# Performance work log

Hardware: AMD Instinct MI355X
Metric: run time of the kernel (lower is better)

## Reference

```python
import jax, jax.numpy as jnp
import numpy as np

E = 65536; N = 10000; LAT = 128; K = 8; OH = 128; GD = 64
M0, M1, M2 = 64, 32, 16                 # multiplicities of 0e, 1o, 2e
D_EDGE = M0 + 3 * M1 + 5 * M2           # 240
NG = M1 + M2                            # 48 gate scalars
O0 = M0 + NG                            # 112 scalar outputs of SO2 (scalars + gates)
C0, C1, C2 = 3 * M0, 3 * M1, 3 * M2     # per-l channels of cat(node, edge, node)
FIN0 = C0 + C1 + C2                     # 336 channels at m=0
FIN1 = C1 + C2                          # 144 channels at |m|=1
FIN2 = C2                               # 48 channels at |m|=2
OUT0 = O0 + M1 + M2                     # 160


def _silu(x):
    return x * jax.nn.sigmoid(x)


def _mlp(x, Ws, bs):
    for i, (W, b) in enumerate(zip(Ws, bs)):
        x = x @ W + b
        if i < len(Ws) - 1:
            x = _silu(x)
    return x


def _split(f):
    # [*, 240] -> scalars [*,64], l1 [*,32,3], l2 [*,16,5]
    return (f[:, :M0],
            f[:, M0:M0 + 3 * M1].reshape(-1, M1, 3),
            f[:, M0 + 3 * M1:].reshape(-1, M2, 5))


def forward(latents, node_features, node_onehot, edge_features, edge_vector,
            cutoff_coeffs, edge_one_hot, wigner_D1, wigner_D2, mole_globals,
            Wg, W0, W1r, W1i, W2r, W2i, P0, b0, P1, P2, We, be, ln_g, ln_b,
            M1W0, M1b0, M1W1, M1b1, M1W2, M1b2,
            M2W0, M2b0, M2W1, M2b1, M2W2, M2b2,
            T0, T1, T2, edge_index, active_edges):
    ec = edge_index[0][active_edges]
    en = edge_index[1][active_edges]
    nc = node_features[ec]
    nnb = node_features[en]
    lat_a = latents[active_edges]

    nc0, nc1, nc2 = _split(nc)
    ef0, ef1, ef2 = _split(edge_features)
    nn0, nn1, nn2 = _split(nnb)
    x0 = jnp.concatenate([nc0, ef0, nn0], 1)          # [E,192]
    x1 = jnp.concatenate([nc1, ef1, nn1], 1)          # [E,96,3]
    x2 = jnp.concatenate([nc2, ef2, nn2], 1)          # [E,48,5]

    # rotate into the edge-aligned frame with cached Wigner D matrices
    y1 = jnp.einsum('eij,ecj->eci', wigner_D1, x1)
    y2 = jnp.einsum('eij,ecj->eci', wigner_D2, x2)

    # expert gates: softmax over routed experts + always-on shared expert
    g = jax.nn.softmax(mole_globals @ Wg, axis=-1)    # [E,K]
    gf = jnp.concatenate([g, jnp.ones((g.shape[0], 1), g.dtype)], 1)  # [E,K+1]

    def moe(f, W):  # f [E,F], W [K+1,F,O] -> gated mixture of expert linears
        return jnp.einsum('eko,ek->eo', jnp.einsum('ef,kfo->eko', f, W), gf)

    # SO(2) linear: independent mixing per |m|
    f0 = jnp.concatenate([x0, y1[:, :, 1], y2[:, :, 2]], 1)   # [E,336]
    o0 = moe(f0, W0)                                          # [E,160]
    o0_s, o0_1, o0_2 = o0[:, :O0], o0[:, O0:O0 + M1], o0[:, O0 + M1:]
    fp1 = jnp.concatenate([y1[:, :, 2], y2[:, :, 3]], 1)      # [E,144]
    fm1 = jnp.concatenate([y1[:, :, 0], y2[:, :, 1]], 1)
    op1 = moe(fp1, W1r) - moe(fm1, W1i)                       # [E,48]
    om1 = moe(fp1, W1i) + moe(fm1, W1r)
    fp2, fm2 = y2[:, :, 4], y2[:, :, 0]                       # [E,48]
    op2 = moe(fp2, W2r) - moe(fm2, W2i)                       # [E,16]
    om2 = moe(fp2, W2i) + moe(fm2, W2r)

    z1 = jnp.stack([om1[:, :M1], o0_1, op1[:, :M1]], -1)      # [E,32,3]
    z2 = jnp.stack([om2, om1[:, M1:], o0_2, op1[:, M1:], op2], -1)  # [E,16,5]
    z1 = jnp.einsum('eji,ecj->eci', wigner_D1, z1)            # rotate back (D^T)
    z2 = jnp.einsum('eji,ecj->eci', wigner_D2, z2)

    # Gate activation: silu scalars, sigmoid gates multiply l>0 parts
    sc = _silu(o0_s[:, :M0])
    gates = jax.nn.sigmoid(o0_s[:, M0:])
    v1 = z1 * gates[:, :M1, None]
    v2 = z2 * gates[:, M1:, None]

    # lin_post: per-l channel mixing, bias on scalars only
    sc = sc @ P0 + b0
    v1 = jnp.einsum('ecm,cd->edm', v1, P1)
    v2 = jnp.einsum('ecm,cd->edm', v2, P2)
    scalars = sc                                              # [E,64]

    # E3ElementLinear: per-channel weights generated from latents
    w = lat_a @ We + be                                       # [E,112]
    sc = sc * w[:, :M0]
    v1 = v1 * w[:, M0:M0 + M1, None]
    v2 = v2 * w[:, M0 + M1:, None]
    new_edge = jnp.concatenate([sc, v1.reshape(-1, 3 * M1), v2.reshape(-1, 5 * M2)], 1)

    # latent update: LN -> MLP1(cat scalars) -> MLP2(cat one-hot) -> cutoff
    mu = lat_a.mean(-1, keepdims=True)
    var = ((lat_a - mu) ** 2).mean(-1, keepdims=True)
    ln = (lat_a - mu) * jax.lax.rsqrt(var + 1e-5) * ln_g + ln_b
    nl = _mlp(jnp.concatenate([ln, scalars], 1), [M1W0, M1W1, M1W2], [M1b0, M1b1, M1b2])
    nl = _mlp(jnp.concatenate([nl, edge_one_hot], 1), [M2W0, M2W1, M2W2], [M2b0, M2b1, M2b2])
    nl = cutoff_coeffs[active_edges][:, None] * nl

    # residual update (identity res since irreps_in == irreps_out)
    upd = jax.nn.sigmoid(jnp.zeros((), new_edge.dtype))
    c_old = jax.lax.rsqrt(upd * upd + 1.0)
    c_new = upd * c_old
    edge_out = c_old * edge_features + c_new * new_edge
    latents = latents.at[active_edges].set(c_new * nl + c_old * lat_a)

    # edge one-hot tensor product (uvu, weighted): per-channel scale from one-hot
    s = 1.0 / jnp.sqrt(jnp.asarray(OH, new_edge.dtype))
    t0 = (edge_one_hot @ T0.T) * s                            # [E,64]
    t1 = (edge_one_hot @ T1.T) * s                            # [E,32]
    t2 = (edge_one_hot @ T2.T) * s                            # [E,16]
    e0, e1, e2 = _split(edge_out)
    oh = jnp.concatenate([e0 * t0,
                          (e1 * t1[:, :, None]).reshape(-1, 3 * M1),
                          (e2 * t2[:, :, None]).reshape(-1, 5 * M2)], 1)
    edge_out = edge_out + oh
    return edge_out, latents, wigner_D1, wigner_D2


def setup_inputs():
    key = jax.random.key(0)
    ks = iter(jax.random.split(key, 64))

    def rn(shape, scale=1.0):
        return jax.random.normal(next(ks), shape, dtype=jnp.float32) * scale

    d = {}
    d['latents'] = rn((E, LAT))
    d['node_features'] = rn((N, D_EDGE))
    d['node_onehot'] = rn((N, GD))
    d['edge_features'] = rn((E, D_EDGE))
    ev = rn((E, 3))
    d['edge_vector'] = ev / jnp.linalg.norm(ev, axis=-1, keepdims=True)
    d['cutoff_coeffs'] = jax.random.uniform(next(ks), (E,), dtype=jnp.float32)
    d['edge_one_hot'] = rn((E, OH))
    d['wigner_D1'] = rn((E, 3, 3), 1.0 / np.sqrt(3))
    d['wigner_D2'] = rn((E, 5, 5), 1.0 / np.sqrt(5))
    d['mole_globals'] = rn((E, GD))
    d['edge_index'] = jax.random.randint(next(ks), (2, E), 0, N, dtype=jnp.int32)
    d['active_edges'] = jnp.arange(E, dtype=jnp.int32)
    # parameters
    d['Wg'] = rn((GD, K), 1.0 / np.sqrt(GD))
    d['W0'] = rn((K + 1, FIN0, OUT0), 1.0 / np.sqrt(FIN0))
    d['W1r'] = rn((K + 1, FIN1, NG), 1.0 / np.sqrt(FIN1))
    d['W1i'] = rn((K + 1, FIN1, NG), 1.0 / np.sqrt(FIN1))
    d['W2r'] = rn((K + 1, FIN2, M2), 1.0 / np.sqrt(FIN2))
    d['W2i'] = rn((K + 1, FIN2, M2), 1.0 / np.sqrt(FIN2))
    d['P0'] = rn((M0, M0), 1.0 / np.sqrt(M0)); d['b0'] = jnp.zeros((M0,), jnp.float32)
    d['P1'] = rn((M1, M1), 1.0 / np.sqrt(M1))
    d['P2'] = rn((M2, M2), 1.0 / np.sqrt(M2))
    d['We'] = rn((LAT, M0 + M1 + M2), 1.0 / np.sqrt(LAT))
    d['be'] = jnp.zeros((M0 + M1 + M2,), jnp.float32)
    d['ln_g'] = jnp.ones((LAT,), jnp.float32); d['ln_b'] = jnp.zeros((LAT,), jnp.float32)
    d['M1W0'] = rn((LAT + M0, 128), 1.0 / np.sqrt(LAT + M0)); d['M1b0'] = jnp.zeros((128,), jnp.float32)
    d['M1W1'] = rn((128, 128), 1.0 / np.sqrt(128)); d['M1b1'] = jnp.zeros((128,), jnp.float32)
    d['M1W2'] = rn((128, LAT), 1.0 / np.sqrt(128)); d['M1b2'] = jnp.zeros((LAT,), jnp.float32)
    d['M2W0'] = rn((LAT + OH, 128), 1.0 / np.sqrt(LAT + OH)); d['M2b0'] = jnp.zeros((128,), jnp.float32)
    d['M2W1'] = rn((128, 128), 1.0 / np.sqrt(128)); d['M2b1'] = jnp.zeros((128,), jnp.float32)
    d['M2W2'] = rn((128, LAT), 1.0 / np.sqrt(128)); d['M2b2'] = jnp.zeros((LAT,), jnp.float32)
    d['T0'] = rn((M0, OH), 1.0 / np.sqrt(OH))
    d['T1'] = rn((M1, OH), 1.0 / np.sqrt(OH))
    d['T2'] = rn((M2, OH), 1.0 / np.sqrt(OH))
    return d


def reference(latents, node_features, node_onehot, edge_features, edge_vector,
              cutoff_coeffs, edge_one_hot, wigner_D1, wigner_D2, mole_globals,
              Wg, W0, W1r, W1i, W2r, W2i, P0, b0, P1, P2, We, be, ln_g, ln_b,
              M1W0, M1b0, M1W1, M1b1, M1W2, M1b2,
              M2W0, M2b0, M2W1, M2b1, M2W2, M2b2,
              T0, T1, T2, edge_index, active_edges):
    return forward(latents, node_features, node_onehot, edge_features, edge_vector,
                   cutoff_coeffs, edge_one_hot, wigner_D1, wigner_D2, mole_globals,
                   Wg, W0, W1r, W1i, W2r, W2i, P0, b0, P1, P2, We, be, ln_g, ln_b,
                   M1W0, M1b0, M1W1, M1b1, M1W2, M1b2,
                   M2W0, M2b0, M2W1, M2b1, M2W2, M2b2,
                   T0, T1, T2, edge_index, active_edges)
```

## Files before the change

### kernel.cpp

```cpp
#include <hip/hip_runtime.h>
#include <hip/hip_bf16.h>
#include <stdint.h>

#define EDGES 65536

typedef unsigned int uint;
typedef unsigned short ushort;
using bf16x8 = __attribute__((ext_vector_type(8))) __bf16;
using f32x4  = __attribute__((ext_vector_type(4))) float;
using uintx4 = __attribute__((ext_vector_type(4))) uint;
using float4v = __attribute__((ext_vector_type(4))) float;
using float2v = __attribute__((ext_vector_type(2))) float;

#define C_OLD 0.8944271909999159f
#define C_NEW 0.4472135954999579f
#define T_SCALE 0.08838834764831845f

__device__ __forceinline__ ushort f2bf(float f) {
  uint x = __builtin_bit_cast(uint, f);
  uint r = x + 0x7FFFu + ((x >> 16) & 1u);
  return (ushort)(r >> 16);
}
__device__ __forceinline__ float bf2f(ushort u) {
  uint x = (uint)u << 16;
  return __builtin_bit_cast(float, x);
}
__device__ __forceinline__ void gload16(const void* g, void* l) {
  __builtin_amdgcn_global_load_lds(
      (const __attribute__((address_space(1))) void*)g,
      (__attribute__((address_space(3))) void*)l, 16, 0, 0);
}

struct PackArgs {
  const float *W0, *W1r, *W1i, *W2r, *W2i;
  const float *s0, *s1, *s2, *s3, *s4, *s5, *we, *t0, *t1, *t2, *p0;
  ushort *B0, *B1, *B2;
  ushort *d0, *d1, *d2, *d3, *d4, *d5, *dwe, *dtt, *dp0;
};
__global__ __launch_bounds__(256) void k_pack(PackArgs p) {
  int bid = blockIdx.x;
  if (bid < 2160) {
    int idx = bid * 256 + threadIdx.x;
    if (idx >= 160 * 3456) return;
    int o = idx / 3456, kf = idx - o * 3456;
    int k = kf / 384, f = kf - k * 384;
    float v = (f < 336) ? p.W0[k * 53760 + f * 160 + o] : 0.f;
    p.B0[idx] = f2bf(v);
  } else if (bid < 3240) {
    int idx = (bid - 2160) * 256 + threadIdx.x;
    if (idx >= 96 * 2880) return;
    int c = idx / 2880, kf = idx - c * 2880;
    int k = kf / 320, f = kf - k * 320;
    float v = 0.f;
    if (f < 288) {
      if (c < 48) v = (f < 144) ? p.W1r[k * 6912 + f * 48 + c] : -p.W1i[k * 6912 + (f - 144) * 48 + c];
      else        v = (f < 144) ? p.W1i[k * 6912 + f * 48 + (c - 48)] : p.W1r[k * 6912 + (f - 144) * 48 + (c - 48)];
    }
    p.B1[idx] = f2bf(v);
  } else if (bid < 3384) {
    int idx = (bid - 3240) * 256 + threadIdx.x;
    if (idx >= 32 * 1152) return;
    int c = idx / 1152, kf = idx - c * 1152;
    int k = kf / 128, f = kf - k * 128;
    float v = 0.f;
    if (f < 96) {
      if (c < 16) v = (f < 48) ? p.W2r[k * 768 + f * 16 + c] : -p.W2i[k * 768 + (f - 48) * 16 + c];
      else        v = (f < 48) ? p.W2i[k * 768 + f * 16 + (c - 16)] : p.W2r[k * 768 + (f - 48) * 16 + (c - 16)];
    }
    p.B2[idx] = f2bf(v);
  } else {
    int idx = (bid - 3384) * 256 + threadIdx.x;
    if (idx < 24576) {
      int n = idx / 192, k = idx - n * 192;
      p.d0[idx] = f2bf(p.s0[k * 128 + n]);
    } else if (idx < 40960) {
      int q = idx - 24576; int n = q >> 7, k = q & 127;
      p.d1[q] = f2bf(p.s1[k * 128 + n]);
    } else if (idx < 57344) {
      int q = idx - 40960; int n = q >> 7, k = q & 127;
      p.d2[q] = f2bf(p.s2[k * 128 + n]);
    } else if (idx < 90112) {
      int q = idx - 57344; int n = q / 256, k = q - n * 256;
      p.d3[q] = f2bf(p.s3[k * 128 + n]);
    } else if (idx < 106496) {
      int q = idx - 90112; int n = q >> 7, k = q & 127;
      p.d4[q] = f2bf(p.s4[k * 128 + n]);
    } else if (idx < 122880) {
      int q = idx - 106496; int n = q >> 7, k = q & 127;
      p.d5[q] = f2bf(p.s5[k * 128 + n]);
    } else if (idx < 139264) {
      int q = idx - 122880; int n = q >> 7, k = q & 127;
      p.dwe[q] = f2bf((n < 112) ? p.we[k * 112 + n] : 0.f);
    } else if (idx < 155648) {
      int q = idx - 139264; int o = q >> 7, h = q & 127;
      float v = 0.f;
      if (o < 64) v = p.t0[o * 128 + h];
      else if (o < 96) v = p.t1[(o - 64) * 128 + h];
      else if (o < 112) v = p.t2[(o - 96) * 128 + h];
      p.dtt[q] = f2bf(v);
    } else if (idx < 159744) {
      int q = idx - 155648; int n = q >> 6, k = q & 63;
      p.dp0[q] = f2bf(p.p0[k * 64 + n]);
    }
  }
}

__global__ __launch_bounds__(256) void k_prep(
    const float* __restrict__ node_f, const float* __restrict__ edge_f,
    const float* __restrict__ D1g, const float* __restrict__ D2g,
    const float* __restrict__ mg_g, const float* __restrict__ Wg,
    const float* __restrict__ latg, const float* __restrict__ eohg,
    const int* __restrict__ eidx, const int* __restrict__ act,
    ushort* __restrict__ f_all, float* __restrict__ gf_out,
    ushort* __restrict__ lat_bf, ushort* __restrict__ mlp2_in) {
  __shared__ float sh[4][1244];
  const int w = threadIdx.x >> 6, lane = threadIdx.x & 63;
  const int e = blockIdx.x * 4 + w;
  float* s = sh[w];
  float* s_nc = s;
  float* s_ef = s + 240;
  float* s_nn = s + 480;
  float* s_d1 = s + 720;
  float* s_d2 = s + 729;
  float* s_mg = s + 754;
  float* s_lg = s + 818;
  ushort* row = (ushort*)(s + 828);
  const int ae = act[e];
  const int ec = eidx[ae], en = eidx[EDGES + ae];
  if (lane < 60) {
    ((float4v*)s_nc)[lane] = ((const float4v*)(node_f + (size_t)ec * 240))[lane];
    ((float4v*)s_ef)[lane] = ((const float4v*)(edge_f + (size_t)e * 240))[lane];
    ((float4v*)s_nn)[lane] = ((const float4v*)(node_f + (size_t)en * 240))[lane];
  }
  if (lane < 9)  s_d1[lane] = D1g[e * 9 + lane];
  if (lane < 25) s_d2[lane] = D2g[e * 25 + lane];
  s_mg[lane] = mg_g[e * 64 + lane];
  {
    const float* lp = latg + (size_t)ae * 128;
    float a0 = lp[2 * lane], a1 = lp[2 * lane + 1];
    ((uint*)lat_bf)[(size_t)e * 64 + lane] = (uint)f2bf(a0) | ((uint)f2bf(a1) << 16);
    const float* ep = eohg + (size_t)e * 128;
    a0 = ep[2 * lane]; a1 = ep[2 * lane + 1];
    ((uint*)mlp2_in)[(size_t)e * 128 + 64 + lane] = (uint)f2bf(a0) | ((uint)f2bf(a1) << 16);
  }
  {
    int k = lane & 7, hg = lane >> 3;
    float a = 0.f;
#pragma unroll
    for (int h = 0; h < 8; ++h) a += s_mg[hg * 8 + h] * Wg[(hg * 8 + h) * 8 + k];
    a += __shfl_xor(a, 8);
    a += __shfl_xor(a, 16);
    a += __shfl_xor(a, 32);
    if (lane < 8) s_lg[lane] = a;
  }
  if (lane < 12) {
    float m = s_lg[0];
    for (int j = 1; j < 8; ++j) m = fmaxf(m, s_lg[j]);
    float den = 0.f;
    for (int j = 0; j < 8; ++j) den += __expf(s_lg[j] - m);
    float v = 0.f;
    if (lane < 8) v = __expf(s_lg[lane] - m) / den;
    else if (lane == 8) v = 1.f;
    gf_out[e * 12 + lane] = v;
  }
  row[lane]       = f2bf(s_nc[lane]);
  row[64 + lane]  = f2bf(s_ef[lane]);
  row[128 + lane] = f2bf(s_nn[lane]);
  if (lane < 48) row[336 + lane] = 0;
  if (lane < 32) { row[672 + lane] = 0; row[800 + lane] = 0; }
#pragma unroll
  for (int it = 0; it < 5; ++it) {
    int q = lane + it * 64;
    if (q < 288) {
      int i = q / 96, c = q - i * 96;
      const float* src = (c < 32) ? s_nc : (c < 64) ? s_ef : s_nn;
      int base = 64 + (c & 31) * 3;
      float v = s_d1[i * 3] * src[base] + s_d1[i * 3 + 1] * src[base + 1] + s_d1[i * 3 + 2] * src[base + 2];
      int dst = (i == 0) ? 528 : (i == 1) ? 192 : 384;
      row[dst + c] = f2bf(v);
    }
  }
#pragma unroll
  for (int it = 0; it < 4; ++it) {
    int q = lane + it * 64;
    if (q < 240) {
      int i = q / 48, c = q - i * 48;
      const float* src = (c < 16) ? s_nc : (c < 32) ? s_ef : s_nn;
      int base = 160 + (c & 15) * 5;
      float v = s_d2[i * 5] * src[base] + s_d2[i * 5 + 1] * src[base + 1] +
                s_d2[i * 5 + 2] * src[base + 2] + s_d2[i * 5 + 3] * src[base + 3] +
                s_d2[i * 5 + 4] * src[base + 4];
      int dst = (i == 0) ? 752 : (i == 1) ? 624 : (i == 2) ? 288 : (i == 3) ? 480 : 704;
      row[dst + c] = f2bf(v);
    }
  }
  const uintx4* row4 = (const uintx4*)row;
  uintx4* dst4 = (uintx4*)(f_all + (size_t)e * 832);
#pragma unroll
  for (int it = 0; it < 2; ++it) {
    int q = lane + it * 64;
    if (q < 104) dst4[q] = row4[q];
  }
}

template <int WAVES, int BM, int KZP, int SPG2, int NGRP, int NCOL, int FOFF, int ASTRIDE,
          bool HASBIAS, int EPI>
__device__ __forceinline__ void gemm_dev(
    int bid, char* sm,
    const ushort* __restrict__ A, const ushort* __restrict__ Bt,
    const float* __restrict__ gf, const float* __restrict__ bias,
    ushort* __restrict__ outb, int ob_stride, int ob_off,
    ushort* __restrict__ outb2) {
  constexpr int T = WAVES * 64;
  constexpr int WRS = WAVES / 2;
  constexpr int RPW = BM / WRS;
  constexpr int MI = RPW / 16;
  constexpr int NFW = NCOL / 32;
  constexpr int A_BYTES = BM * 128;
  constexpr int B_BYTES = NCOL * 128;
  constexpr int NT2 = KZP / 64;
  constexpr int AI = (BM * 8) / T;
  constexpr int NB = NCOL * 8;
  constexpr int BI = (NB + T - 1) / T;
  static_assert(NCOL % 32 == 0 && KZP % 64 == 0 && RPW % 16 == 0 && (BM * 8) % T == 0, "geom");
  const int tid = threadIdx.x;
  const int lane = tid & 63, wid = tid >> 6;
  const int wr = wid >> 1, wc = wid & 1;
  const int g16 = lane >> 4;
  const int lane15 = lane & 15;
  const int e0 = bid * BM;
  const f32x4 vzero = {0.f, 0.f, 0.f, 0.f};

  const char* bSrc[BI];
#pragma unroll
  for (int it = 0; it < BI; ++it) {
    int q = tid + it * T;
    if (q < NB) {
      int c = q >> 3, ch = (q & 7) ^ (c & 7);
      bSrc[it] = (const char*)(Bt + (size_t)c * KZP) + ch * 16;
    } else bSrc[it] = nullptr;
  }

  f32x4 accS[MI][NFW];
#pragma unroll
  for (int mi = 0; mi < MI; ++mi)
#pragma unroll
    for (int n = 0; n < NFW; ++n) accS[mi][n] = vzero;

  if constexpr (NGRP > 1) {
    char* b_lds = sm;
    f32x4 accC[MI][NFW];
#pragma unroll
    for (int mi = 0; mi < MI; ++mi)
#pragma unroll
      for (int n = 0; n < NFW; ++n) accC[mi][n] = vzero;

    float gfr[MI][4];
    auto gf_pref = [&](int gx) {
#pragma unroll
      for (int mi = 0; mi < MI; ++mi)
#pragma unroll
        for (int j = 0; j < 4; ++j)
          gfr[mi][j] = gf[(size_t)(e0 + wr * RPW + mi * 16 + g16 * 4 + j) * 12 + gx];
    };
    gf_pref(0);

    bf16x8 afr[SPG2][MI][2];
#pragma unroll
    for (int wi = 0; wi < SPG2; ++wi)
#pragma unroll
      for (int mi = 0; mi < MI; ++mi)
#pragma unroll
        for (int s = 0; s < 2; ++s)
          afr[wi][mi][s] = *(const bf16x8*)(
              A + (size_t)(e0 + wr * RPW + mi * 16 + lane15) * ASTRIDE + FOFF +
              wi * 64 + s * 32 + g16 * 8);

    auto stageB = [&](int t2, int buf) {
#pragma unroll
      for (int it = 0; it < BI; ++it) {
        int q = tid + it * T;
        if (q < NB)
          gload16(bSrc[it] + (size_t)t2 * 128, b_lds + buf * B_BYTES + (tid - lane + it * T) * 16);
      }
    };

    stageB(0, 0);
    __syncthreads();
    int cur = 0;
    for (int g = 0; g < NGRP; ++g) {
#pragma unroll
      for (int wi = 0; wi < SPG2; ++wi) {
        int t2 = g * SPG2 + wi;
        if (t2 + 1 < NT2) stageB(t2 + 1, cur ^ 1);
        const char* bL = b_lds + cur * B_BYTES;
#pragma unroll
        for (int s = 0; s < 2; ++s) {
#pragma unroll
          for (int n = 0; n < NFW; ++n) {
            int cB = (wc * NFW + n) * 16 + lane15;
            int slot = (s * 4 + g16) ^ (cB & 7);
            bf16x8 b = *(const bf16x8*)(bL + cB * 128 + slot * 16);
#pragma unroll
            for (int mi = 0; mi < MI; ++mi)
              accC[mi][n] = __builtin_amdgcn_mfma_f32_16x16x32_bf16(afr[wi][mi][s], b, accC[mi][n], 0, 0, 0);
          }
        }
        if (wi == SPG2 - 1) {
#pragma unroll
          for (int mi = 0; mi < MI; ++mi)
#pragma unroll
            for (int n = 0; n < NFW; ++n) {
#pragma unroll
              for (int j = 0; j < 4; ++j) accS[mi][n][j] += gfr[mi][j] * accC[mi][n][j];
              accC[mi][n] = vzero;
            }
          if (g + 1 < NGRP) gf_pref(g + 1);
        }
        __syncthreads();
        cur ^= 1;
      }
    }
  } else {
    char* a_lds = sm;
    char* b_lds = sm + 2 * A_BYTES;
    const char* aSrc[AI];
#pragma unroll
    for (int it = 0; it < AI; ++it) {
      int q = tid + it * T;
      int r = q >> 3, ch = (q & 7) ^ (r & 7);
      aSrc[it] = (const char*)(A + (size_t)(e0 + r) * ASTRIDE + FOFF) + ch * 16;
    }
    auto stage = [&](int t2, int buf) {
#pragma unroll
      for (int it = 0; it < AI; ++it)
        gload16(aSrc[it] + t2 * 128, a_lds + buf * A_BYTES + (tid - lane + it * T) * 16);
#pragma unroll
      for (int it = 0; it < BI; ++it) {
        int q = tid + it * T;
        if (q < NB)
          gload16(bSrc[it] + t2 * 128, b_lds + buf * B_BYTES + (tid - lane + it * T) * 16);
      }
    };
    stage(0, 0);
    __syncthreads();
    int cur = 0;
    for (int t2 = 0; t2 < NT2; ++t2) {
      if (t2 + 1 < NT2) stage(t2 + 1, cur ^ 1);
      const char* aL = a_lds + cur * A_BYTES;
      const char* bL = b_lds + cur * B_BYTES;
#pragma unroll
      for (int s = 0; s < 2; ++s) {
        bf16x8 a[MI];
#pragma unroll
        for (int mi = 0; mi < MI; ++mi) {
          int rA = wr * RPW + mi * 16 + lane15;
          int slot = (s * 4 + g16) ^ (rA & 7);
          a[mi] = *(const bf16x8*)(aL + rA * 128 + slot * 16);
        }
#pragma unroll
        for (int n = 0; n < NFW; ++n) {
          int cB = (wc * NFW + n) * 16 + lane15;
          int slot = (s * 4 + g16) ^ (cB & 7);
          bf16x8 b = *(const bf16x8*)(bL + cB * 128 + slot * 16);
#pragma unroll
          for (int mi = 0; mi < MI; ++mi)
            accS[mi][n] = __builtin_amdgcn_mfma_f32_16x16x32_bf16(a[mi], b, accS[mi][n], 0, 0, 0);
        }
      }
      __syncthreads();
      cur ^= 1;
    }
  }

#pragma unroll
  for (int mi = 0; mi < MI; ++mi) {
    const int row0 = wr * RPW + mi * 16 + g16 * 4;
#pragma unroll
    for (int n = 0; n < NFW; ++n) {
      const int c = (wc * NFW + n) * 16 + lane15;
      float bv = 0.f;
      if constexpr (HASBIAS) bv = bias[c];
#pragma unroll
      for (int j = 0; j < 4; ++j) {
        float v = accS[mi][n][j] + bv;
        const int er = e0 + row0 + j;
        if constexpr (EPI == 1) v = v / (1.f + __expf(-v));
        outb[(size_t)er * ob_stride + ob_off + c] = f2bf(v);
        if constexpr (EPI == 2) {
          if ((wc * NFW + n) * 16 < 64)
            outb2[(size_t)er * 256 + c] = f2bf(v / (1.f + __expf(-v)));
        }
      }
    }
  }
}

struct MoeArgs {
  const ushort *f_all, *B0t, *B1t, *B2t;
  const float* gfb;
  ushort *moeout, *m2in;
};
__global__ __launch_bounds__(512) void k_moe(MoeArgs a) {
  __shared__ char sm[2 * 160 * 128 + 16];
  int bid = blockIdx.x;
  if (bid < 512) {
    gemm_dev<8, 128, 3456, 6, 9, 160, 0, 832, false, 2>(
        bid, sm, a.f_all, a.B0t, a.gfb, nullptr, a.moeout, 288, 0, a.m2in);
  } else if (bid < 1024) {
    gemm_dev<8, 128, 2880, 5, 9, 96, 384, 832, false, 0>(
        bid - 512, sm, a.f_all, a.B1t, a.gfb, nullptr, a.moeout, 288, 160, nullptr);
  } else {
    gemm_dev<8, 128, 1152, 2, 9, 32, 704, 832, false, 0>(
        bid - 1024, sm, a.f_all, a.B2t, a.gfb, nullptr, a.moeout, 288, 256, nullptr);
  }
}

struct Small3Args {
  const ushort *latbf, *Wet, *m2in, *Ttb, *P0t;
  const float* b0;
  ushort *wbuf, *tbuf, *m1in;
};
__global__ __launch_bounds__(256) void k_small3(Small3Args a) {
  __shared__ char sm[49168];
  int bid = blockIdx.x;
  if (bid < 1024) {
    gemm_dev<4, 64, 128, 1, 1, 128, 0, 128, false, 0>(
        bid, sm, a.latbf, a.Wet, nullptr, nullptr, a.wbuf, 128, 0, nullptr);
  } else if (bid < 2048) {
    gemm_dev<4, 64, 128, 1, 1, 128, 128, 256, false, 0>(
        bid - 1024, sm, a.m2in, a.Ttb, nullptr, nullptr, a.tbuf, 128, 0, nullptr);
  } else {
    gemm_dev<4, 64, 64, 1, 1, 64, 0, 256, true, 0>(
        bid - 2048, sm, a.m2in, a.P0t, nullptr, a.b0, a.m1in, 192, 128, nullptr);
  }
}

struct MlpArgs {
  const ushort *m1in, *m2in, *Wt1, *Wt2, *Wt3, *Wt4, *Wt5, *Wt6;
  const float *b1, *b2, *b3, *b4, *b5, *b6;
  const int* act;
  const float *cutg, *latg;
  float* out_lat;
};
__global__ __launch_bounds__(256) void k_mlp(MlpArgs A) {
  __shared__ char sm[61440];
  char* Xa = sm;
  char* Xb = sm + 12288;
  char* Xe = sm + 20480;
  char* W0 = sm + 28672;
  char* W1 = sm + 45056;
  const int tid = threadIdx.x;
  const int lane = tid & 63, w = tid >> 6;
  const int wr = w >> 1, wc = w & 1;
  const int lane15 = lane & 15, g16 = lane >> 4;
  const int e32 = blockIdx.x * 32;
  const f32x4 vzero = {0.f, 0.f, 0.f, 0.f};

  auto stage_w = [&](const ushort* Wt, int K2, int t2, char* dst) {
#pragma unroll
    for (int it = 0; it < 4; ++it) {
      int q = tid + it * 256;
      int c = q >> 3, ch = (q & 7) ^ (c & 7);
      gload16((const char*)Wt + (size_t)c * K2 + t2 * 128 + ch * 16,
              dst + (w + it * 4) * 1024);
    }
  };
  {
#pragma unroll
    for (int it = 0; it < 3; ++it) {
      int q = tid + it * 256;
      int r = q / 24, c24 = q - r * 24;
      int t2 = c24 >> 3, ch = (c24 & 7) ^ (r & 7);
      gload16((const char*)A.m1in + (size_t)(e32 + r) * 384 + t2 * 128 + ch * 16,
              Xa + (w + it * 4) * 1024);
    }
#pragma unroll
    for (int it = 0; it < 2; ++it) {
      int q = tid + it * 256;
      int r = q >> 4, c16 = q & 15;
      int t2 = c16 >> 3, ch = (c16 & 7) ^ (r & 7);
      gload16((const char*)A.m2in + (size_t)(e32 + r) * 512 + 256 + t2 * 128 + ch * 16,
              Xe + (w + it * 4) * 1024);
    }
  }
  stage_w(A.Wt1, 384, 0, W0);
  __syncthreads();

  f32x4 acc[4];
#pragma unroll
  for (int n = 0; n < 4; ++n) acc[n] = vzero;

  auto compute = [&](const char* xin, int xstride, int t2loc, const char* wl) {
#pragma unroll
    for (int s = 0; s < 2; ++s) {
      int row = wr * 16 + lane15;
      bf16x8 a = *(const bf16x8*)(xin + row * xstride + t2loc * 128 + (((s * 4 + g16) ^ (row & 7)) << 4));
#pragma unroll
      for (int n = 0; n < 4; ++n) {
        int cB = wc * 64 + n * 16 + lane15;
        bf16x8 b = *(const bf16x8*)(wl + cB * 128 + (((s * 4 + g16) ^ (cB & 7)) << 4));
        acc[n] = __builtin_amdgcn_mfma_f32_16x16x32_bf16(a, b, acc[n], 0, 0, 0);
      }
    }
  };
  auto epi_x = [&](const float* bias, char* xout, int xstride, bool dosilu) {
#pragma unroll
    for (int n = 0; n < 4; ++n) {
      int c = wc * 64 + n * 16 + lane15;
      float bv = bias[c];
      int ch = (n * 16 + lane15) >> 3;
#pragma unroll
      for (int j = 0; j < 4; ++j) {
        int row = wr * 16 + g16 * 4 + j;
        float v = acc[n][j] + bv;
        if (dosilu) v = v / (1.f + __expf(-v));
        *(ushort*)(xout + row * xstride + wc * 128 + ((ch ^ (row & 7)) << 4) + ((lane15 & 7) << 1)) = f2bf(v);
      }
      acc[n] = vzero;
    }
  };

  stage_w(A.Wt1, 384, 1, W1); compute(Xa, 384, 0, W0); __syncthreads();
  stage_w(A.Wt1, 384, 2, W0); compute(Xa, 384, 1, W1); __syncthreads();
  stage_w(A.Wt2, 256, 0, W1); compute(Xa, 384, 2, W0); epi_x(A.b1, Xb, 256, true); __syncthreads();
  stage_w(A.Wt2, 256, 1, W0); compute(Xb, 256, 0, W1); __syncthreads();
  stage_w(A.Wt3, 256, 0, W1); compute(Xb, 256, 1, W0); epi_x(A.b2, Xa, 384, true); __syncthreads();
  stage_w(A.Wt3, 256, 1, W0); compute(Xa, 384, 0, W1); __syncthreads();
  stage_w(A.Wt4, 512, 0, W1); compute(Xa, 384, 1, W0); epi_x(A.b3, Xb, 256, false); __syncthreads();
  stage_w(A.Wt4, 512, 1, W0); compute(Xb, 256, 0, W1); __syncthreads();
  stage_w(A.Wt4, 512, 2, W1); compute(Xb, 256, 1, W0); __syncthreads();
  stage_w(A.Wt4, 512, 3, W0); compute(Xe, 256, 0, W1); __syncthreads();
  stage_w(A.Wt5, 256, 0, W1); compute(Xe, 256, 1, W0); epi_x(A.b4, Xa, 384, true); __syncthreads();
  stage_w(A.Wt5, 256, 1, W0); compute(Xa, 384, 0, W1); __syncthreads();
  stage_w(A.Wt6, 256, 0, W1); compute(Xa, 384, 1, W0); epi_x(A.b5, Xb, 256, true); __syncthreads();
  stage_w(A.Wt6, 256, 1, W0); compute(Xb, 256, 0, W1); __syncthreads();
  compute(Xb, 256, 1, W0);
#pragma unroll
  for (int n = 0; n < 4; ++n) {
    int c = wc * 64 + n * 16 + lane15;
    float bv = A.b6[c];
#pragma unroll
    for (int j = 0; j < 4; ++j) {
      int row = wr * 16 + g16 * 4 + j;
      int er = e32 + row;
      int ae = A.act[er];
      float v = acc[n][j] + bv;
      A.out_lat[(size_t)ae * 128 + c] = C_NEW * A.cutg[ae] * v + C_OLD * A.latg[(size_t)ae * 128 + c];
    }
  }
}

__global__ __launch_bounds__(512) void k_postf(
    const ushort* __restrict__ moeout,
    const float* __restrict__ D1g, const float* __restrict__ D2g,
    const float* __restrict__ latg, const int* __restrict__ act,
    const float* __restrict__ P1, const float* __restrict__ P2,
    const ushort* __restrict__ wbuf, const float* __restrict__ beg,
    const float* __restrict__ lng, const float* __restrict__ lnb,
    const ushort* __restrict__ tbufp, const float* __restrict__ efg,
    ushort* __restrict__ m1in, float* __restrict__ out_edge) {
  __shared__ float SM[1136 + 8 * 920];
  ushort* Btab = (ushort*)SM;
  float* be_s = SM + 768;
  float* lng_s = SM + 880;
  float* lnb_s = SM + 1008;
  const int t = threadIdx.x;
  const int w = t >> 6, lane = t & 63;
  float* Wp = SM + 1136 + w * 920;
  float* o   = Wp;
  float* row = Wp + 224;
  float* sg  = Wp + 464;
  float* d1  = Wp + 512;
  float* d2  = Wp + 524;
  ushort* wvh = (ushort*)(Wp + 552);
  ushort* tvh = (ushort*)(Wp + 608);
  ushort* tile = (ushort*)(Wp + 664);
  const int e = blockIdx.x * 8 + w;
  const int ae = act[e];
  const f32x4 vzero = {0.f, 0.f, 0.f, 0.f};

  float ef[4];
  ef[0] = efg[(size_t)e * 240 + lane];
  ef[1] = efg[(size_t)e * 240 + 64 + lane];
  ef[2] = efg[(size_t)e * 240 + 128 + lane];
  ef[3] = (lane < 48) ? efg[(size_t)e * 240 + 192 + lane] : 0.f;
  float2v ll = ((const float2v*)(latg + (size_t)ae * 128))[lane];

  if (lane < 28) {
    uintx4 raw = *(const uintx4*)(moeout + (size_t)e * 288 + 64 + lane * 8);
    float* dst = o + lane * 8;
#pragma unroll
    for (int j = 0; j < 4; ++j) {
      uint u = raw[j];
      dst[2 * j] = bf2f((ushort)(u & 0xFFFF));
      dst[2 * j + 1] = bf2f((ushort)(u >> 16));
    }
  }
  if (lane < 14) {
    *(uintx4*)((char*)wvh + lane * 16) = *(const uintx4*)(wbuf + (size_t)e * 128 + lane * 8);
    *(uintx4*)((char*)tvh + lane * 16) = *(const uintx4*)(tbufp + (size_t)e * 128 + lane * 8);
  }
  if (lane < 8) {
    uintx4 raw = *(const uintx4*)(m1in + (size_t)e * 192 + 128 + lane * 8);
    float* dst = row + lane * 8;
#pragma unroll
    for (int j = 0; j < 4; ++j) {
      uint u = raw[j];
      dst[2 * j] = bf2f((ushort)(u & 0xFFFF));
      dst[2 * j + 1] = bf2f((ushort)(u >> 16));
    }
  }
  if (lane < 9)  d1[lane] = D1g[(size_t)e * 9 + lane];
  if (lane < 25) d2[lane] = D2g[(size_t)e * 25 + lane];
  if (lane < 48) sg[lane] = 1.f / (1.f + __expf(-o[lane]));

#pragma unroll
  for (int i = 0; i < 3; ++i) {
    int q = t + i * 512;
    int tbl = q >> 9, idx = q & 511;
    int d = idx >> 5, c = idx & 31;
    float v;
    if (tbl == 0) v = P1[c * 32 + d];
    else if (tbl == 1) v = P1[c * 32 + 16 + d];
    else v = (c < 16) ? P2[c * 16 + d] : 0.f;
    Btab[tbl * 512 + d * 32 + (((c >> 3) ^ (d & 3)) << 3) + (c & 7)] = f2bf(v);
  }
  if (t < 368) {
    if (t < 112) be_s[t] = beg[t];
    else if (t < 240) lng_s[t - 112] = lng[t - 112];
    else lnb_s[t - 240] = lnb[t - 240];
  }

  float sum = ll[0] + ll[1];
  float sq = ll[0] * ll[0] + ll[1] * ll[1];
#pragma unroll
  for (int m = 32; m > 0; m >>= 1) {
    sum += __shfl_xor(sum, m);
    sq += __shfl_xor(sq, m);
  }
  const float mu = sum * (1.f / 128.f);
  const float rs = rsqrtf(sq * (1.f / 128.f) - mu * mu + 1e-5f);

  __syncthreads();

  {
    int i = 2 * lane;
    float l0 = (ll[0] - mu) * rs * lng_s[i] + lnb_s[i];
    float l1 = (ll[1] - mu) * rs * lng_s[i + 1] + lnb_s[i + 1];
    ((uint*)m1in)[(size_t)e * 96 + lane] = (uint)f2bf(l0) | ((uint)f2bf(l1) << 16);
  }
#pragma unroll
  for (int rr = 0; rr < 2; ++rr) {
    int r = lane + rr * 64;
    if (r < 96) {
      int m = r >> 5, c = r & 31;
      float v = d1[m] * o[144 + c] + d1[3 + m] * o[48 + c] + d1[6 + m] * o[96 + c];
      tile[m * 32 + (((c >> 3) ^ (m & 3)) << 3) + (c & 7)] = f2bf(v * sg[c]);
    }
  }
#pragma unroll
  for (int rr = 0; rr < 3; ++rr) {
    int r = lane + rr * 64;
    if (r < 160) {
      int rw = 3 + (r >> 5), c = r & 31;
      ushort hv = 0;
      if (c < 16) {
        int m = rw - 3;
        float v = d2[m] * o[208 + c] + d2[5 + m] * o[176 + c] + d2[10 + m] * o[80 + c] +
                  d2[15 + m] * o[128 + c] + d2[20 + m] * o[192 + c];
        hv = f2bf(v * sg[32 + c]);
      }
      tile[rw * 32 + (((c >> 3) ^ (rw & 3)) << 3) + (c & 7)] = hv;
    }
  }
  {
    const int r15 = lane & 15, g = lane >> 4;
    const int fslot = (g ^ (r15 & 3)) << 3;
    bf16x8 afr = *(const bf16x8*)(tile + r15 * 32 + fslot);
    bf16x8 b1a = *(const bf16x8*)(Btab + r15 * 32 + fslot);
    bf16x8 b1b = *(const bf16x8*)(Btab + 512 + r15 * 32 + fslot);
    bf16x8 b2p = *(const bf16x8*)(Btab + 1024 + r15 * 32 + fslot);
    f32x4 v1a = __builtin_amdgcn_mfma_f32_16x16x32_bf16(afr, b1a, vzero, 0, 0, 0);
    f32x4 v1b = __builtin_amdgcn_mfma_f32_16x16x32_bf16(afr, b1b, vzero, 0, 0, 0);
    f32x4 v2r = __builtin_amdgcn_mfma_f32_16x16x32_bf16(afr, b2p, vzero, 0, 0, 0);
    if (g == 0) {
      float s1 = bf2f(wvh[64 + r15]) + be_s[64 + r15];
      row[64 + r15 * 3 + 0] = v1a[0] * s1;
      row[64 + r15 * 3 + 1] = v1a[1] * s1;
      row[64 + r15 * 3 + 2] = v1a[2] * s1;
      float s2 = bf2f(wvh[80 + r15]) + be_s[80 + r15];
      row[64 + (16 + r15) * 3 + 0] = v1b[0] * s2;
      row[64 + (16 + r15) * 3 + 1] = v1b[1] * s2;
      row[64 + (16 + r15) * 3 + 2] = v1b[2] * s2;
      float s3 = bf2f(wvh[96 + r15]) + be_s[96 + r15];
      row[160 + r15 * 5 + 0] = v2r[3] * s3;
    } else if (g == 1) {
      float s3 = bf2f(wvh[96 + r15]) + be_s[96 + r15];
      row[160 + r15 * 5 + 1] = v2r[0] * s3;
      row[160 + r15 * 5 + 2] = v2r[1] * s3;
      row[160 + r15 * 5 + 3] = v2r[2] * s3;
      row[160 + r15 * 5 + 4] = v2r[3] * s3;
    }
  }
  row[lane] = row[lane] * (bf2f(wvh[lane]) + be_s[lane]);
#pragma unroll
  for (int r = 0; r < 4; ++r) {
    int d = lane + r * 64;
    if (r < 3 || lane < 48) {
      float v = C_OLD * ef[r] + C_NEW * row[d];
      int ti = (d < 64) ? d : (d < 160) ? 64 + (d - 64) / 3 : 96 + (d - 160) / 5;
      float f = bf2f(tvh[ti]) * T_SCALE;
      out_edge[(size_t)e * 240 + d] = v * (1.f + f);
    }
  }
}

extern "C" void kernel_launch(void* const* d_in, const int* in_sizes, int n_in,
                              void* d_out, int out_size, void* d_ws, size_t ws_size,
                              hipStream_t stream) {
  const float* latents = (const float*)d_in[0];
  const float* node_f  = (const float*)d_in[1];
  const float* edge_f  = (const float*)d_in[3];
  const float* cutoff  = (const float*)d_in[5];
  const float* eoh     = (const float*)d_in[6];
  const float* D1      = (const float*)d_in[7];
  const float* D2      = (const float*)d_in[8];
  const float* mg      = (const float*)d_in[9];
  const int*   eidx    = (const int*)d_in[10];
  const int*   act     = (const int*)d_in[11];
  const float* Wg      = (const float*)d_in[12];
  const float* W0      = (const float*)d_in[13];
  const float* W1r     = (const float*)d_in[14];
  const float* W1i     = (const float*)d_in[15];
  const float* W2r     = (const float*)d_in[16];
  const float* W2i     = (const float*)d_in[17];
  const float* P0      = (const float*)d_in[18];
  const float* b0      = (const float*)d_in[19];
  const float* P1      = (const float*)d_in[20];
  const float* P2      = (const float*)d_in[21];
  const float* We      = (const float*)d_in[22];
  const float* be      = (const float*)d_in[23];
  const float* lng     = (const float*)d_in[24];
  const float* lnb     = (const float*)d_in[25];
  const float* M1W0_   = (const float*)d_in[26];
  const float* M1b0_   = (const float*)d_in[27];
  const float* M1W1_   = (const float*)d_in[28];
  const float* M1b1_   = (const float*)d_in[29];
  const float* M1W2_   = (const float*)d_in[30];
  const float* M1b2_   = (const float*)d_in[31];
  const float* M2W0_   = (const float*)d_in[32];
  const float* M2b0_   = (const float*)d_in[33];
  const float* M2W1_   = (const float*)d_in[34];
  const float* M2b1_   = (const float*)d_in[35];
  const float* M2W2_   = (const float*)d_in[36];
  const float* M2b2_   = (const float*)d_in[37];
  const float* T0      = (const float*)d_in[38];
  const float* T1      = (const float*)d_in[39];
  const float* T2      = (const float*)d_in[40];

  float* out_edge = (float*)d_out;
  float* out_lat  = out_edge + (size_t)EDGES * 240;
  float* out_d1   = out_lat + (size_t)EDGES * 128;
  float* out_d2   = out_d1 + (size_t)EDGES * 9;

  char* ws = (char*)d_ws;
  size_t off = 0;
  auto alloc = [&](size_t bytes) -> char* {
    char* p = ws + off;
    off += (bytes + 255) & ~size_t(255);
    return p;
  };
  ushort* f_all  = (ushort*)alloc((size_t)EDGES * 832 * 2);
  float*  gfb    = (float*) alloc((size_t)EDGES * 12 * 4);
  ushort* moeout = (ushort*)alloc((size_t)EDGES * 288 * 2);
  ushort* m2in   = (ushort*)alloc((size_t)EDGES * 256 * 2);
  ushort* latbf  = (ushort*)alloc((size_t)EDGES * 128 * 2);
  ushort* wbuf   = (ushort*)alloc((size_t)EDGES * 128 * 2);
  ushort* B0t    = (ushort*)alloc(160 * 3456 * 2);
  ushort* B1t    = (ushort*)alloc(96 * 2880 * 2);
  ushort* B2t    = (ushort*)alloc(32 * 1152 * 2);
  ushort* Wt1    = (ushort*)alloc(128 * 192 * 2);
  ushort* Wt2    = (ushort*)alloc(128 * 128 * 2);
  ushort* Wt3    = (ushort*)alloc(128 * 128 * 2);
  ushort* Wt4    = (ushort*)alloc(128 * 256 * 2);
  ushort* Wt5    = (ushort*)alloc(128 * 128 * 2);
  ushort* Wt6    = (ushort*)alloc(128 * 128 * 2);
  ushort* Wet    = (ushort*)alloc(128 * 128 * 2);
  ushort* Ttb    = (ushort*)alloc(128 * 128 * 2);
  ushort* P0t    = (ushort*)alloc(64 * 64 * 2);

  ushort* m1in = f_all;
  ushort* tbuf = latbf;

  hipMemcpyAsync(out_d1, (const void*)D1, (size_t)EDGES * 9 * 4, hipMemcpyDeviceToDevice, stream);
  hipMemcpyAsync(out_d2, (const void*)D2, (size_t)EDGES * 25 * 4, hipMemcpyDeviceToDevice, stream);

  if (ws_size < off) return;

  PackArgs pk = {W0, W1r, W1i, W2r, W2i,
                 M1W0_, M1W1_, M1W2_, M2W0_, M2W1_, M2W2_, We, T0, T1, T2, P0,
                 B0t, B1t, B2t,
                 Wt1, Wt2, Wt3, Wt4, Wt5, Wt6, Wet, Ttb, P0t};
  k_pack<<<4008, 256, 0, stream>>>(pk);

  k_prep<<<EDGES / 4, 256, 0, stream>>>(node_f, edge_f, D1, D2, mg, Wg, latents, eoh,
                                        eidx, act, f_all, gfb, latbf, m2in);

  MoeArgs mo = {f_all, B0t, B1t, B2t, gfb, moeout, m2in};
  k_moe<<<1536, 512, 0, stream>>>(mo);

  Small3Args s3 = {latbf, Wet, m2in, Ttb, P0t, b0, wbuf, tbuf, m1in};
  k_small3<<<3072, 256, 0, stream>>>(s3);

  k_postf<<<EDGES / 8, 512, 0, stream>>>(moeout, D1, D2, latents, act, P1, P2,
                                         wbuf, be, lng, lnb, tbuf, edge_f, m1in, out_edge);

  MlpArgs ma = {m1in, m2in, Wt1, Wt2, Wt3, Wt4, Wt5, Wt6,
                M1b0_, M1b1_, M1b2_, M2b0_, M2b1_, M2b2_,
                act, cutoff, latents, out_lat};
  k_mlp<<<EDGES / 32, 256, 0, stream>>>(ma);
}
```

Baseline: 437.1 us.

## Fold latent and T projection GEMMs into the MoE kernel launch

Moves the two 128x128 projection GEMMs (latents·We and m2in·T) out of the small-GEMM kernel and into the MoE kernel as extra blocks, retiled to 128-row, 8-warp blocks. Only the bias GEMM that depends on MoE output stays in a separate small kernel. tbuf gets its own workspace buffer instead of aliasing latbf, since latbf is now read concurrently. The goal is to fill the tail of the MoE launch and cut launch and serialization cost. The trade-off is that the MoE kernel's static LDS grows to 64KB, which may reduce its occupancy.

After: 434.8 us. About the same (-0.5%).

```diff
diff --git a/kernel.cpp b/kernel.cpp
--- a/kernel.cpp
+++ b/kernel.cpp
@@ -397,43 +397,40 @@
 }
 
 struct MoeArgs {
-  const ushort *f_all, *B0t, *B1t, *B2t;
+  const ushort *f_all, *B0t, *B1t, *B2t, *latbf, *Wet, *m2in, *Ttb;
   const float* gfb;
-  ushort *moeout, *m2in;
+  ushort *moeout, *m2out, *wbuf, *tbuf;
 };
 __global__ __launch_bounds__(512) void k_moe(MoeArgs a) {
-  __shared__ char sm[2 * 160 * 128 + 16];
+  __shared__ char sm[65552];
   int bid = blockIdx.x;
   if (bid < 512) {
     gemm_dev<8, 128, 3456, 6, 9, 160, 0, 832, false, 2>(
-        bid, sm, a.f_all, a.B0t, a.gfb, nullptr, a.moeout, 288, 0, a.m2in);
+        bid, sm, a.f_all, a.B0t, a.gfb, nullptr, a.moeout, 288, 0, a.m2out);
   } else if (bid < 1024) {
     gemm_dev<8, 128, 2880, 5, 9, 96, 384, 832, false, 0>(
         bid - 512, sm, a.f_all, a.B1t, a.gfb, nullptr, a.moeout, 288, 160, nullptr);
-  } else {
+  } else if (bid < 1536) {
     gemm_dev<8, 128, 1152, 2, 9, 32, 704, 832, false, 0>(
         bid - 1024, sm, a.f_all, a.B2t, a.gfb, nullptr, a.moeout, 288, 256, nullptr);
-  }
-}
-
-struct Small3Args {
-  const ushort *latbf, *Wet, *m2in, *Ttb, *P0t;
+  } else if (bid < 2048) {
+    gemm_dev<8, 128, 128, 1, 1, 128, 0, 128, false, 0>(
+        bid - 1536, sm, a.latbf, a.Wet, nullptr, nullptr, a.wbuf, 128, 0, nullptr);
+  } else {
+    gemm_dev<8, 128, 128, 1, 1, 128, 128, 256, false, 0>(
+        bid - 2048, sm, a.m2in, a.Ttb, nullptr, nullptr, a.tbuf, 128, 0, nullptr);
+  }
+}
+
+struct SpsArgs {
+  const ushort *m2in, *P0t;
   const float* b0;
-  ushort *wbuf, *tbuf, *m1in;
+  ushort* m1in;
 };
-__global__ __launch_bounds__(256) void k_small3(Small3Args a) {
+__global__ __launch_bounds__(256) void k_sps(SpsArgs a) {
   __shared__ char sm[49168];
-  int bid = blockIdx.x;
-  if (bid < 1024) {
-    gemm_dev<4, 64, 128, 1, 1, 128, 0, 128, false, 0>(
-        bid, sm, a.latbf, a.Wet, nullptr, nullptr, a.wbuf, 128, 0, nullptr);
-  } else if (bid < 2048) {
-    gemm_dev<4, 64, 128, 1, 1, 128, 128, 256, false, 0>(
-        bid - 1024, sm, a.m2in, a.Ttb, nullptr, nullptr, a.tbuf, 128, 0, nullptr);
-  } else {
-    gemm_dev<4, 64, 64, 1, 1, 64, 0, 256, true, 0>(
-        bid - 2048, sm, a.m2in, a.P0t, nullptr, a.b0, a.m1in, 192, 128, nullptr);
-  }
+  gemm_dev<4, 64, 64, 1, 1, 64, 0, 256, true, 0>(
+      blockIdx.x, sm, a.m2in, a.P0t, nullptr, a.b0, a.m1in, 192, 128, nullptr);
 }
 
 struct MlpArgs {
@@ -777,6 +774,7 @@
   ushort* m2in   = (ushort*)alloc((size_t)EDGES * 256 * 2);
   ushort* latbf  = (ushort*)alloc((size_t)EDGES * 128 * 2);
   ushort* wbuf   = (ushort*)alloc((size_t)EDGES * 128 * 2);
+  ushort* tbufb  = (ushort*)alloc((size_t)EDGES * 128 * 2);
   ushort* B0t    = (ushort*)alloc(160 * 3456 * 2);
   ushort* B1t    = (ushort*)alloc(96 * 2880 * 2);
   ushort* B2t    = (ushort*)alloc(32 * 1152 * 2);
@@ -791,7 +789,6 @@
   ushort* P0t    = (ushort*)alloc(64 * 64 * 2);
 
   ushort* m1in = f_all;
-  ushort* tbuf = latbf;
 
   hipMemcpyAsync(out_d1, (const void*)D1, (size_t)EDGES * 9 * 4, hipMemcpyDeviceToDevice, stream);
   hipMemcpyAsync(out_d2, (const void*)D2, (size_t)EDGES * 25 * 4, hipMemcpyDeviceToDevice, stream);
@@ -807,14 +804,15 @@
   k_prep<<<EDGES / 4, 256, 0, stream>>>(node_f, edge_f, D1, D2, mg, Wg, latents, eoh,
                                         eidx, act, f_all, gfb, latbf, m2in);
 
-  MoeArgs mo = {f_all, B0t, B1t, B2t, gfb, moeout, m2in};
-  k_moe<<<1536, 512, 0, stream>>>(mo);
-
-  Small3Args s3 = {latbf, Wet, m2in, Ttb, P0t, b0, wbuf, tbuf, m1in};
-  k_small3<<<3072, 256, 0, stream>>>(s3);
+  MoeArgs mo = {f_all, B0t, B1t, B2t, latbf, Wet, m2in, Ttb, gfb,
+                moeout, m2in, wbuf, tbufb};
+  k_moe<<<2560, 512, 0, stream>>>(mo);
+
+  SpsArgs sp = {m2in, P0t, b0, m1in};
+  k_sps<<<1024, 256, 0, stream>>>(sp);
 
   k_postf<<<EDGES / 8, 512, 0, stream>>>(moeout, D1, D2, latents, act, P1, P2,
-                                         wbuf, be, lng, lnb, tbuf, edge_f, m1in, out_edge);
+                                         wbuf, be, lng, lnb, tbufb, edge_f, m1in, out_edge);
 
   MlpArgs ma = {m1in, m2in, Wt1, Wt2, Wt3, Wt4, Wt5, Wt6,
                 M1b0_, M1b1_, M1b2_, M2b0_, M2b1_, M2b2_,
```

## Triple-buffer B tiles in MoE GEMM with fine-grained vmcnt waits

Applied to the files above, without the earlier changes.

Turns the double-buffered B-tile staging in the register-resident-A GEMM path into a triple-buffered pipeline that prefetches two tiles ahead. The full __syncthreads is replaced by an s_waitcnt vmcnt that waits only for the older load group, followed by a raw s_barrier. The aim is to hide global-to-LDS load latency behind the MFMA work. In exchange k_moe uses more shared memory (3x160x128 bytes), which may lower occupancy, and the hand-counted vmcnt logic must stay correct for each instantiation.

After: 420.6 us. -3.8%, faster.

```diff
diff --git a/kernel.cpp b/kernel.cpp
--- a/kernel.cpp
+++ b/kernel.cpp
@@ -29,6 +29,13 @@
   __builtin_amdgcn_global_load_lds(
       (const __attribute__((address_space(1))) void*)g,
       (__attribute__((address_space(3))) void*)l, 16, 0, 0);
+}
+template <int N> __device__ __forceinline__ void wait_vm() {
+  if constexpr (N <= 0) asm volatile("s_waitcnt vmcnt(0)" ::: "memory");
+  else if constexpr (N == 1) asm volatile("s_waitcnt vmcnt(1)" ::: "memory");
+  else if constexpr (N == 2) asm volatile("s_waitcnt vmcnt(2)" ::: "memory");
+  else if constexpr (N == 3) asm volatile("s_waitcnt vmcnt(3)" ::: "memory");
+  else asm volatile("s_waitcnt vmcnt(4)" ::: "memory");
 }
 
 struct PackArgs {
@@ -285,15 +292,30 @@
       }
     };
 
+    constexpr int FULLI = NB / T;
+    constexpr int PARTW = (NB % T) / 64;
+    auto wait_tail = [&](bool issued) {
+      if (!issued) { wait_vm<0>(); return; }
+      if constexpr ((NB % T) == 0) {
+        wait_vm<FULLI>();
+      } else {
+        if (wid < PARTW) wait_vm<FULLI + 1>(); else wait_vm<FULLI>();
+      }
+    };
+
     stageB(0, 0);
-    __syncthreads();
-    int cur = 0;
+    stageB(1, 1);
+    wait_tail(true);
+    __builtin_amdgcn_s_barrier();
+    asm volatile("" ::: "memory");
+
     for (int g = 0; g < NGRP; ++g) {
 #pragma unroll
       for (int wi = 0; wi < SPG2; ++wi) {
         int t2 = g * SPG2 + wi;
-        if (t2 + 1 < NT2) stageB(t2 + 1, cur ^ 1);
-        const char* bL = b_lds + cur * B_BYTES;
+        bool issue = (t2 + 2) < NT2;
+        if (issue) stageB(t2 + 2, (t2 + 2) % 3);
+        const char* bL = b_lds + (t2 % 3) * B_BYTES;
 #pragma unroll
         for (int s = 0; s < 2; ++s) {
 #pragma unroll
@@ -317,8 +339,9 @@
             }
           if (g + 1 < NGRP) gf_pref(g + 1);
         }
-        __syncthreads();
-        cur ^= 1;
+        wait_tail(issue);
+        __builtin_amdgcn_s_barrier();
+        asm volatile("" ::: "memory");
       }
     }
   } else {
@@ -402,7 +425,7 @@
   ushort *moeout, *m2in;
 };
 __global__ __launch_bounds__(512) void k_moe(MoeArgs a) {
-  __shared__ char sm[2 * 160 * 128 + 16];
+  __shared__ char sm[3 * 160 * 128 + 16];
   int bid = blockIdx.x;
   if (bid < 512) {
     gemm_dev<8, 128, 3456, 6, 9, 160, 0, 832, false, 2>(
```
